# Optimization experiments

Measured on AMD Instinct MI355X. Metric: run time of the kernel, lower is better.

Reference implementation:

```python
import jax, jax.numpy as jnp
import numpy as np
from jax import lax

NUM_HOP = 2      # opt.num_hop
POOL_HOP = 1     # Encoder(..., num_hop=1) in gnn_pools
K_POOL = 1024    # int(pooling_ratio * num_patches) = 0.5 * 2048
TH = 0.0         # opt.nonzero_th
T = 0.07         # NCE temperature
NEG_FILL = -10.0


def l2norm(x):
    # Normalize(power=2): x / (sum(x^2, dim=1, keepdim)^(1/2))
    return x / jnp.sqrt(jnp.sum(x * x, axis=1, keepdims=True))


def tagconv(A, h, W, b, k):
    # DGL TAGConv: concat_{i=0..k} (D^-1/2 A D^-1/2)^i h, then linear
    deg = jnp.sum(A, axis=1)
    dinv = lax.rsqrt(jnp.maximum(deg, 1e-12))
    An = A * dinv[:, None] * dinv[None, :]   # [N,N] normalized adjacency
    feats = [h]
    for _ in range(k):
        h = An @ h
        feats.append(h)
    return jnp.concatenate(feats, axis=1) @ W + b


def nce_pair(f_t, f_s):
    # calc_gnn NCE: positives = diag(f_t . f_s); negatives = full gram with diag masked to -10
    n = f_t.shape[0]
    eye = jnp.eye(n, dtype=bool)
    pos = jnp.sum(f_t * f_s, axis=1, keepdims=True)          # [N,1]
    neg_s = jnp.where(eye, NEG_FILL, f_t @ f_s.T)            # [N,N]
    neg_t = jnp.where(eye, NEG_FILL, f_s @ f_t.T)
    out_s = jnp.concatenate([pos, neg_s], axis=1) / T
    out_t = jnp.concatenate([pos, neg_t], axis=1) / T
    # CrossEntropy with label 0 == -log_softmax(out)[:, 0], mean over rows
    loss_s = -jnp.mean(jax.nn.log_softmax(out_s, axis=1)[:, 0])
    loss_t = -jnp.mean(jax.nn.log_softmax(out_t, axis=1)[:, 0])
    return loss_s + loss_t


def setup_inputs() -> dict:
    key = jax.random.key(0)
    ks = jax.random.split(key, 8)
    N, C, D = 2048, 512, 128
    g = 0.02  # init_gain ('normal' init)
    return {
        "fs": jax.random.normal(ks[0], (N, C), jnp.float32),
        "ft": jax.random.normal(ks[1], (N, C), jnp.float32),
        "W_embed": g * jax.random.normal(ks[2], (C, D), jnp.float32),
        "b_embed": jnp.zeros((D,), jnp.float32),
        "W_gnn": g * jax.random.normal(ks[3], ((NUM_HOP + 1) * D, D), jnp.float32),
        "b_gnn": jnp.zeros((D,), jnp.float32),
        "W_pool": g * jax.random.normal(ks[4], (D, 1), jnp.float32),
        "b_pool": jnp.zeros((1,), jnp.float32),
        "W_gnnp": g * jax.random.normal(ks[5], ((POOL_HOP + 1) * D, D), jnp.float32),
        "b_gnnp": jnp.zeros((D,), jnp.float32),
    }


def reference(fs, ft, W_embed, b_embed, W_gnn, b_gnn, W_pool, b_pool, W_gnnp, b_gnnp):
    # Embed: linear + l2 norm
    f_es = l2norm(fs @ W_embed + b_embed)   # student [N, nc]
    f_et = l2norm(ft @ W_embed + b_embed)   # teacher [N, nc]

    # nonzero_graph on detached teacher features; same adjacency reused for student
    ft_d = lax.stop_gradient(f_et)
    n = f_et.shape[0]
    eye = jnp.eye(n, dtype=bool)
    A = (ft_d @ ft_d.T > TH).astype(f_et.dtype)
    A = jnp.where(eye, 1.0, A)  # dgl.add_self_loop

    # TAGConv encoder + l2norm; teacher branch detached
    f_gt = lax.stop_gradient(l2norm(tagconv(A, f_et, W_gnn, b_gnn, NUM_HOP)))
    f_gs = l2norm(tagconv(A, f_es, W_gnn, b_gnn, NUM_HOP))
    loss_g = nce_pair(f_gt, f_gs)

    # Pool / top_k_graph
    scores = jax.nn.sigmoid((f_gt @ W_pool + b_pool)[:, 0])   # [N]
    vals, idx = lax.top_k(scores, K_POOL)
    new_ht = f_gt[idx] * vals[:, None]
    new_hs = f_gs[idx] * vals[:, None]
    un = (A > 0).astype(A.dtype)
    un2 = ((un @ un) > 0).astype(A.dtype)        # 2-hop boolean adjacency
    sub = un2[idx][:, idx]                       # [k,k]
    deg = jnp.sum(sub, axis=1)
    g_pool = sub / deg[None, :]                  # replicates torch broadcast in norm_g(g/degrees)

    # pooled-stage Encoder (TAGConv k=1) on the pooled graph structure (with self loops)
    k = K_POOL
    eye_k = jnp.eye(k, dtype=bool)
    Ap = (g_pool > 0).astype(A.dtype)
    Ap = jnp.where(eye_k, 1.0, Ap)
    f_pt = lax.stop_gradient(l2norm(tagconv(Ap, new_ht, W_gnnp, b_gnnp, POOL_HOP)))
    f_ps = l2norm(tagconv(Ap, new_hs, W_gnnp, b_gnnp, POOL_HOP))
    loss_pool = nce_pair(f_pt, f_ps)

    return loss_g + loss_pool
```

## Files before the change

### kernel.cpp

```cpp
#include <hip/hip_runtime.h>


#define TINV (1.0f / 0.07f)

using short8 = __attribute__((ext_vector_type(8))) short;
using f32x4  = __attribute__((ext_vector_type(4))) float;

__device__ __forceinline__ unsigned short f2bf(float f) {
    unsigned u = __float_as_uint(f);
    u += 0x7fff + ((u >> 16) & 1);
    return (unsigned short)(u >> 16);
}

template<bool BT>
__device__ __forceinline__ void mm_tile(const float* __restrict__ A, int lda,
                                        const float* __restrict__ B, int ldb,
                                        int i0, int j0, int k0, int k1,
                                        float (&acc)[4][4],
                                        float (&As)[16][68], float (&Bs)[16][68])
{
    const int tid = threadIdx.x;
    const int tx = tid & 15;
    const int ty = tid >> 4;
    const int lr = tid >> 2;
    const int lc = (tid & 3) * 4;
    for (int k = k0; k < k1; k += 16) {
        float4 av = *(const float4*)(A + (size_t)(i0 + lr) * lda + (k + lc));
        As[lc + 0][lr] = av.x; As[lc + 1][lr] = av.y;
        As[lc + 2][lr] = av.z; As[lc + 3][lr] = av.w;
        if (BT) {
            float4 bv = *(const float4*)(B + (size_t)(j0 + lr) * ldb + (k + lc));
            Bs[lc + 0][lr] = bv.x; Bs[lc + 1][lr] = bv.y;
            Bs[lc + 2][lr] = bv.z; Bs[lc + 3][lr] = bv.w;
        } else {
            const int n = tid & 63;
            const int kb = tid >> 6;
#pragma unroll
            for (int it = 0; it < 4; ++it)
                Bs[kb * 4 + it][n] = B[(size_t)(k + kb * 4 + it) * ldb + (j0 + n)];
        }
        __syncthreads();
#pragma unroll
        for (int kk = 0; kk < 16; ++kk) {
            float a[4], b[4];
#pragma unroll
            for (int u = 0; u < 4; ++u) a[u] = As[kk][ty * 4 + u];
#pragma unroll
            for (int v = 0; v < 4; ++v) b[v] = Bs[kk][tx * 4 + v];
#pragma unroll
            for (int u = 0; u < 4; ++u)
#pragma unroll
                for (int v = 0; v < 4; ++v)
                    acc[u][v] = fmaf(a[u], b[v], acc[u][v]);
        }
        __syncthreads();
    }
}

__device__ __forceinline__ void mm64x128(const unsigned short* __restrict__ Ab, int lda,
                                         const unsigned short* __restrict__ Bb, int ldb,
                                         int i0, int j0, int k0, int Kc,
                                         f32x4 (&acc)[8],
                                         unsigned short (&As)[64][40],
                                         unsigned short (&Bs)[128][40])
{
    const int tid = threadIdx.x;
    const int w = tid >> 6;
    const int lane = tid & 63;
    const int m = lane & 15;
    const int q = lane >> 4;
    const int ar = tid >> 2;
    const int ac = (tid & 3) * 8;
    for (int ks = 0; ks < Kc; ks += 32) {
        const int k = k0 + ks;
        *(ulonglong2*)&As[ar][ac] =
            *(const ulonglong2*)(Ab + (size_t)(i0 + ar) * lda + k + ac);
        *(ulonglong2*)&Bs[ar][ac] =
            *(const ulonglong2*)(Bb + (size_t)(j0 + ar) * ldb + k + ac);
        *(ulonglong2*)&Bs[ar + 64][ac] =
            *(const ulonglong2*)(Bb + (size_t)(j0 + ar + 64) * ldb + k + ac);
        __syncthreads();
        short8 a = *(const short8*)&As[w * 16 + m][q * 8];
#pragma unroll
        for (int nt = 0; nt < 8; ++nt) {
            short8 b = *(const short8*)&Bs[nt * 16 + m][q * 8];
            acc[nt] = __builtin_amdgcn_mfma_f32_16x16x32_bf16(a, b, acc[nt], 0, 0, 0);
        }
        __syncthreads();
    }
}

__launch_bounds__(256)
__global__ void k_setup_embed(const float* __restrict__ fs, const float* __restrict__ ft,
                              const float* __restrict__ W, float* __restrict__ part,
                              size_t zstr, int* __restrict__ zwords, int zcount,
                              float* __restrict__ out,
                              const float* __restrict__ Wg, const float* __restrict__ Wp,
                              unsigned short* __restrict__ Wtall)
{
    __shared__ float As[16][68];
    __shared__ float Bs[16][68];
    const int b = blockIdx.x;
    const int tid = threadIdx.x;
    if (b < 512) {
        const int z = b & 3;
        const int by = (b >> 2) & 63;
        const int bx = b >> 8;
        const float* A = (by < 32) ? ft : fs;
        const int i0 = (by & 31) * 64;
        const int j0 = bx * 64;
        float acc[4][4] = {};
        mm_tile<false>(A, 512, W, 128, i0, j0, z * 128, z * 128 + 128, acc, As, Bs);
        const int tx = tid & 15, ty = tid >> 4;
        float* dst = part + (size_t)z * zstr;
#pragma unroll
        for (int u = 0; u < 4; ++u) {
            const size_t ri = (size_t)(by * 64 + ty * 4 + u) * 128 + j0 + tx * 4;
            float4 vv;
            vv.x = acc[u][0]; vv.y = acc[u][1]; vv.z = acc[u][2]; vv.w = acc[u][3];
            *(float4*)(dst + ri) = vv;
        }
    } else if (b < 561) {
        const int i = (b - 512) * 256 + tid;
        if (i < zcount) zwords[i] = 0;
        if (b == 512 && tid == 0) out[0] = 0.0f;
    } else {
        const int e0 = (b - 561) * 2048 + tid;
#pragma unroll
        for (int it = 0; it < 8; ++it) {
            const int e = e0 + it * 256;
            const int c = e >> 14;
            const int rem = e & 16383;
            const int n = rem >> 7, k = rem & 127;
            const float* src = (c < 3) ? (Wg + (size_t)c * 16384)
                                       : (Wp + (size_t)(c - 3) * 16384);
            Wtall[e] = f2bf(src[(size_t)k * 128 + n]);
        }
    }
}

__global__ void combine_norm(const float* __restrict__ part, int nz, size_t zstr,
                             const float* __restrict__ bias,
                             float* __restrict__ f32out,
                             unsigned short* __restrict__ bf16out)
{
    const int row = blockIdx.x;
    const int tid = threadIdx.x;
    float v = bias[tid];
    for (int z = 0; z < nz; ++z) v += part[(size_t)z * zstr + (size_t)row * 128 + tid];
    __shared__ float red[128];
    red[tid] = v * v;
    __syncthreads();
    for (int s = 64; s > 0; s >>= 1) {
        if (tid < s) red[tid] += red[tid + s];
        __syncthreads();
    }
    const float o = v * (1.0f / sqrtf(red[0]));
    f32out[(size_t)row * 128 + tid] = o;
    bf16out[(size_t)row * 128 + tid] = f2bf(o);
}

__launch_bounds__(256)
__global__ void k_gram_fused(const float* __restrict__ f_e,
                             unsigned short* __restrict__ A01,
                             unsigned long long* __restrict__ bits,
                             int* __restrict__ deg,
                             const unsigned short* __restrict__ feb,
                             const unsigned short* __restrict__ Wt,
                             float* __restrict__ hW)
{
    __shared__ __align__(16) unsigned char smem[15360];
    const int b = blockIdx.x;
    const int tid = threadIdx.x;
    if (b >= 528) {
        unsigned short (&As2)[64][40]  = *reinterpret_cast<unsigned short(*)[64][40]>(smem);
        unsigned short (&Bs2)[128][40] = *reinterpret_cast<unsigned short(*)[128][40]>(smem + 5120);
        const int lb = b - 528;
        const int z = lb >> 6;
        const int i0 = (lb & 63) * 64;
        f32x4 acc[8];
#pragma unroll
        for (int t = 0; t < 8; ++t)
#pragma unroll
            for (int r = 0; r < 4; ++r) acc[t][r] = 0.0f;
        mm64x128(feb, 128, Wt + (size_t)z * 16384, 128, i0, 0, 0, 128, acc, As2, Bs2);
        const int w = tid >> 6, lane = tid & 63, m = lane & 15, q = lane >> 4;
        float* Cb = hW + (size_t)z * (4096ull * 128);
#pragma unroll
        for (int nt = 0; nt < 8; ++nt) {
            const int col = nt * 16 + m;
#pragma unroll
            for (int r = 0; r < 4; ++r) {
                const int row = i0 + w * 16 + q * 4 + r;
                Cb[(size_t)row * 128 + col] = acc[nt][r];
            }
        }
        return;
    }
    float (&As)[16][68] = *reinterpret_cast<float(*)[16][68]>(smem);
    float (&Bs)[16][68] = *reinterpret_cast<float(*)[16][68]>(smem + 4352);
    unsigned char (&nib)[64][16]  = *reinterpret_cast<unsigned char(*)[64][16]>(smem + 8704);
    unsigned char (&nibT)[64][16] = *reinterpret_cast<unsigned char(*)[64][16]>(smem + 9728);
    unsigned long long (&chk)[64]  = *reinterpret_cast<unsigned long long(*)[64]>(smem + 10752);
    unsigned long long (&chkT)[64] = *reinterpret_cast<unsigned long long(*)[64]>(smem + 11264);
    int by = (int)((sqrtf(8.0f * b + 1.0f) - 1.0f) * 0.5f);
    while ((by + 1) * (by + 2) / 2 <= b) ++by;
    while (by * (by + 1) / 2 > b) --by;
    const int bx = b - by * (by + 1) / 2;
    const int i0 = by * 64, j0 = bx * 64;
    float acc[4][4] = {};
    mm_tile<true>(f_e, 128, f_e, 128, i0, j0, 0, 128, acc, As, Bs);
    const int tx = tid & 15, ty = tid >> 4;
    unsigned pb = 0;
#pragma unroll
    for (int u = 0; u < 4; ++u)
#pragma unroll
        for (int v = 0; v < 4; ++v) {
            bool pred = (acc[u][v] > 0.0f) || (i0 + ty * 4 + u == j0 + tx * 4 + v);
            pb |= (unsigned)pred << (u * 4 + v);
        }
#pragma unroll
    for (int u = 0; u < 4; ++u) nib[ty * 4 + u][tx] = (pb >> (4 * u)) & 15;
#pragma unroll
    for (int v = 0; v < 4; ++v) {
        unsigned nt = 0;
#pragma unroll
        for (int u = 0; u < 4; ++u) nt |= ((pb >> (u * 4 + v)) & 1u) << u;
        nibT[tx * 4 + v][ty] = nt;
    }
    __syncthreads();
    if (tid < 64) {
        unsigned long long c = 0;
#pragma unroll
        for (int t = 0; t < 16; ++t) c |= (unsigned long long)nib[tid][t] << (4 * t);
        chk[tid] = c;
        bits[(size_t)(i0 + tid) * 32 + (j0 >> 6)] = c;
        atomicAdd(&deg[i0 + tid], __popcll(c));
    } else if (tid < 128 && bx != by) {
        const int r = tid - 64;
        unsigned long long c = 0;
#pragma unroll
        for (int t = 0; t < 16; ++t) c |= (unsigned long long)nibT[r][t] << (4 * t);
        chkT[r] = c;
        bits[(size_t)(j0 + r) * 32 + (i0 >> 6)] = c;
        atomicAdd(&deg[j0 + r], __popcll(c));
    }
    __syncthreads();
#pragma unroll
    for (int it = 0; it < 4; ++it) {
        const int row = it * 16 + (tid >> 4);
        const int c0 = (tid & 15) * 4;
        unsigned short o[4];
#pragma unroll
        for (int c = 0; c < 4; ++c)
            o[c] = ((chk[row] >> (c0 + c)) & 1) ? (unsigned short)0x3F80 : (unsigned short)0;
        *(ulonglong1*)&A01[(size_t)(i0 + row) * 2048 + j0 + c0] = *(ulonglong1*)o;
        if (bx != by) {
            unsigned short o2[4];
#pragma unroll
            for (int c = 0; c < 4; ++c)
                o2[c] = ((chkT[row] >> (c0 + c)) & 1) ? (unsigned short)0x3F80 : (unsigned short)0;
            *(ulonglong1*)&A01[(size_t)(j0 + row) * 2048 + i0 + c0] = *(ulonglong1*)o2;
        }
    }
}

__launch_bounds__(256)
__global__ void mm_bf16(const unsigned short* __restrict__ A, int lda, size_t aZ,
                        const unsigned short* __restrict__ B, int ldb, size_t bZ,
                        float* __restrict__ C, int ldc, size_t cZ,
                        int Kc, int kZ)
{
    __shared__ unsigned short As[64][40];
    __shared__ unsigned short Bs[128][40];
    const int tid = threadIdx.x;
    const int bz = blockIdx.z;
    const int i0 = blockIdx.y * 64;
    const int j0 = blockIdx.x * 128;
    const int k0 = bz * kZ;
    const unsigned short* Ab = A + (size_t)bz * aZ;
    const unsigned short* Bb = B + (size_t)bz * bZ;
    float* Cb = C + (size_t)bz * cZ;
    f32x4 acc[8];
#pragma unroll
    for (int t = 0; t < 8; ++t)
#pragma unroll
        for (int r = 0; r < 4; ++r) acc[t][r] = 0.0f;
    mm64x128(Ab, lda, Bb, ldb, i0, j0, k0, Kc, acc, As, Bs);
    const int w = tid >> 6, lane = tid & 63, m = lane & 15, q = lane >> 4;
#pragma unroll
    for (int nt = 0; nt < 8; ++nt) {
        const int col = j0 + nt * 16 + m;
#pragma unroll
        for (int r = 0; r < 4; ++r) {
            const int row = i0 + w * 16 + q * 4 + r;
            Cb[(size_t)row * ldc + col] = acc[nt][r];
        }
    }
}

__global__ void reduce_xt(const float* __restrict__ part, int nz, size_t zstr,
                          int M, const float* __restrict__ dinv,
                          const float* __restrict__ addT,
                          unsigned short* __restrict__ xt)
{
    __shared__ float T[32][33];
    const int tid = threadIdx.x;
    const int iloc = tid >> 3, nq = (tid & 7) * 4;
    const int n = blockIdx.x * 32 + nq;
    const int i = blockIdx.y * 32 + iloc;
    float4 s = *(const float4*)(part + (size_t)i * 256 + n);
    for (int z = 1; z < nz; ++z) {
        float4 t = *(const float4*)(part + (size_t)z * zstr + (size_t)i * 256 + n);
        s.x += t.x; s.y += t.y; s.z += t.z; s.w += t.w;
    }
    const float d = dinv[i];
    const int srow = (n >= 128 ? M : 0) + i;
    float4 a = *(const float4*)(addT + (size_t)srow * 128 + (n & 127));
    T[nq + 0][iloc] = (a.x + s.x * d) * d;
    T[nq + 1][iloc] = (a.y + s.y * d) * d;
    T[nq + 2][iloc] = (a.z + s.z * d) * d;
    T[nq + 3][iloc] = (a.w + s.w * d) * d;
    __syncthreads();
    const int nloc = tid >> 3, ic = (tid & 7) * 4;
    unsigned short o2[4];
#pragma unroll
    for (int c = 0; c < 4; ++c) o2[c] = f2bf(T[nloc][ic + c]);
    *(ulonglong1*)(xt + (size_t)(blockIdx.x * 32 + nloc) * M + blockIdx.y * 32 + ic) =
        *(ulonglong1*)o2;
}

__global__ void combine_tag(const float* __restrict__ part, int nz, size_t zstr,
                            int Mnodes,
                            const float* __restrict__ add,
                            const float* __restrict__ dinv,
                            const float* __restrict__ bias,
                            float* __restrict__ f32out,
                            unsigned short* __restrict__ bf16out,
                            const float* __restrict__ Wp, const float* __restrict__ bp,
                            float* __restrict__ scores)
{
    const int row = blockIdx.x;
    const int tid = threadIdx.x;
    const int node = (row < Mnodes) ? row : row - Mnodes;
    const int boff = (row < Mnodes) ? 0 : 128;
    float s = 0.0f;
    for (int z = 0; z < nz; ++z)
        s += part[(size_t)z * zstr + (size_t)node * 256 + boff + tid];
    float v = bias[tid] + add[(size_t)row * 128 + tid] + dinv[node] * s;
    __shared__ float red[128];
    red[tid] = v * v;
    __syncthreads();
    for (int st = 64; st > 0; st >>= 1) {
        if (tid < st) red[tid] += red[tid + st];
        __syncthreads();
    }
    const float o = v * (1.0f / sqrtf(red[0]));
    if (f32out) f32out[(size_t)row * 128 + tid] = o;
    bf16out[(size_t)row * 128 + tid] = f2bf(o);
    if (Wp && row < Mnodes) {
        __syncthreads();
        red[tid] = o * Wp[tid];
        __syncthreads();
        for (int st = 64; st > 0; st >>= 1) {
            if (tid < st) red[tid] += red[tid + st];
            __syncthreads();
        }
        if (tid == 0) scores[row] = 1.0f / (1.0f + expf(-(red[0] + bp[0])));
    }
}

__global__ void make_xt(const float* __restrict__ src, const int* __restrict__ deg,
                        unsigned short* __restrict__ xt, float* __restrict__ dinv)
{
    __shared__ float T[32][33];
    const int b = blockIdx.x;
    const int bx = b & 7, by = b >> 3;
    const int tid = threadIdx.x;
    const int iloc = tid >> 3, nq = (tid & 7) * 4;
    const int n0 = bx * 32;
    const int i = by * 32 + iloc;
    const int srow = (n0 >= 128 ? 2048 : 0) + i;
    float4 f = *(const float4*)(src + (size_t)srow * 128 + ((n0 + nq) & 127));
    const float d = 1.0f / sqrtf((float)deg[i]);
    if (bx == 0 && (tid & 7) == 0) dinv[i] = d;
    T[nq + 0][iloc] = f.x * d; T[nq + 1][iloc] = f.y * d;
    T[nq + 2][iloc] = f.z * d; T[nq + 3][iloc] = f.w * d;
    __syncthreads();
    const int nloc = tid >> 3, ic = (tid & 7) * 4;
    unsigned short o[4];
#pragma unroll
    for (int c = 0; c < 4; ++c) o[c] = f2bf(T[nloc][ic + c]);
    *(ulonglong1*)(xt + (size_t)(n0 + nloc) * 2048 + by * 32 + ic) = *(ulonglong1*)o;
}

__launch_bounds__(256)
__global__ void k_nce_topk(const unsigned short* __restrict__ A,
                           const unsigned short* __restrict__ B,
                           float* __restrict__ rowsum, float* __restrict__ colsum,
                           float* __restrict__ pos, int gramBlocks, int bw,
                           const float* __restrict__ scores,
                           float* __restrict__ vals, int* __restrict__ idx)
{
    __shared__ unsigned short As[64][40];
    __shared__ unsigned short Bs[128][40];
    __shared__ float colbuf[4][128];
    __shared__ unsigned sv[2048];
    __shared__ int hist[256];
    __shared__ int shp, shr, sh_base, sh_out, wsum[5];
    const int tid = threadIdx.x;
    const int b = blockIdx.x;
    if (b < gramBlocks) {
        const int bx = b % bw, by = b / bw;
        const int i0 = by * 64;
        const int j0 = bx * 128;
        const int w = tid >> 6;
        const int lane = tid & 63;
        const int m = lane & 15;
        const int q = lane >> 4;
        f32x4 acc[8];
#pragma unroll
        for (int t = 0; t < 8; ++t)
#pragma unroll
            for (int r = 0; r < 4; ++r) acc[t][r] = 0.0f;
        mm64x128(A, 128, B, 128, i0, j0, 0, 128, acc, As, Bs);
        float rpart[4] = {0.0f, 0.0f, 0.0f, 0.0f};
        float cpart[8];
#pragma unroll
        for (int nt = 0; nt < 8; ++nt) {
            const int col = j0 + nt * 16 + m;
            float cs = 0.0f;
#pragma unroll
            for (int r = 0; r < 4; ++r) {
                const int row = i0 + w * 16 + q * 4 + r;
                float g = acc[nt][r];
                float e = __expf(g * TINV);
                if (row == col) { pos[row] = g; e = 0.0f; }
                rpart[r] += e;
                cs += e;
            }
            cpart[nt] = cs;
        }
#pragma unroll
        for (int r = 0; r < 4; ++r) {
            float v = rpart[r];
            v += __shfl_xor(v, 1); v += __shfl_xor(v, 2);
            v += __shfl_xor(v, 4); v += __shfl_xor(v, 8);
            if (m == 0) atomicAdd(&rowsum[i0 + w * 16 + q * 4 + r], v);
        }
#pragma unroll
        for (int nt = 0; nt < 8; ++nt) {
            float v = cpart[nt];
            v += __shfl_xor(v, 16); v += __shfl_xor(v, 32);
            if (q == 0) colbuf[w][nt * 16 + m] = v;
        }
        __syncthreads();
        if (tid < 128) {
            float v = colbuf[0][tid] + colbuf[1][tid] + colbuf[2][tid] + colbuf[3][tid];
            atomicAdd(&colsum[j0 + tid], v);
        }
    } else {
        for (int e = tid; e < 2048; e += 256) sv[e] = __float_as_uint(scores[e]);
        if (tid == 0) { shp = 0; shr = 1024; sh_base = 0; sh_out = 0; }
        __syncthreads();
        for (int byte = 3; byte >= 0; --byte) {
            hist[tid] = 0;
            __syncthreads();
            const unsigned pref = (unsigned)shp;
            const unsigned pmask = (byte == 3) ? 0u : (0xFFFFFFFFu << ((byte + 1) * 8));
            for (int e = tid; e < 2048; e += 256) {
                unsigned u = sv[e];
                if ((u & pmask) == (pref & pmask))
                    atomicAdd(&hist[(u >> (byte * 8)) & 255], 1);
            }
            __syncthreads();
            if (tid == 0) {
                int rem = shr, bs = 255;
                for (; bs > 0; --bs) {
                    if (hist[bs] >= rem) break;
                    rem -= hist[bs];
                }
                shp = (int)(pref | ((unsigned)bs << (byte * 8)));
                shr = rem;
            }
            __syncthreads();
        }
        const unsigned t = (unsigned)shp;
        const int remain = shr;
        const int lane = tid & 63, wave = tid >> 6;
        for (int pass = 0; pass < 8; ++pass) {
            const int e = pass * 256 + tid;
            const unsigned u = sv[e];
            const bool eq = (u == t);
            unsigned long long mk = __ballot(eq);
            int wpre = __popcll(mk & ((1ull << lane) - 1ull));
            if (lane == 0) wsum[wave] = __popcll(mk);
            __syncthreads();
            if (tid == 0) {
                int a = sh_base;
                for (int ww = 0; ww < 4; ++ww) { int c = wsum[ww]; wsum[ww] = a; a += c; }
                sh_base = a;
            }
            __syncthreads();
            const int rank = eq ? (wsum[wave] + wpre) : 0x7fffffff;
            if ((u > t) || (eq && rank < remain)) {
                int slot = atomicAdd(&sh_out, 1);
                idx[slot] = e;
                vals[slot] = __uint_as_float(u);
            }
            __syncthreads();
        }
    }
}

__global__ void k_final_ap(const float* __restrict__ rs, const float* __restrict__ cs,
                           const float* __restrict__ pos, float* __restrict__ out,
                           const unsigned long long* __restrict__ bits,
                           const int* __restrict__ idx,
                           unsigned short* __restrict__ Ap, int* __restrict__ degp)
{
    __shared__ unsigned long long pb[32][33];
    __shared__ unsigned long long qb[32][33];
    __shared__ float red[256];
    const int b = blockIdx.x;
    const int tid = threadIdx.x;
    if (b < 1024) {
        const int tp = (b >> 5) * 32;
        const int tq = (b & 31) * 32;
        for (int t = tid; t < 1024; t += 256) {
            int r = t >> 5, w = t & 31;
            pb[r][w] = bits[(size_t)idx[tp + r] * 32 + w];
            qb[r][w] = bits[(size_t)idx[tq + r] * 32 + w];
        }
        __syncthreads();
        const int pi = tid >> 3;
        const int qc0 = (tid & 7) * 4;
        unsigned long long a0 = 0, a1 = 0, a2 = 0, a3 = 0;
#pragma unroll
        for (int w = 0; w < 32; ++w) {
            const unsigned long long p = pb[pi][w];
            a0 |= p & qb[qc0 + 0][w];
            a1 |= p & qb[qc0 + 1][w];
            a2 |= p & qb[qc0 + 2][w];
            a3 |= p & qb[qc0 + 3][w];
        }
        unsigned short o[4] = { (unsigned short)(a0 ? 0x3F80 : 0),
                                (unsigned short)(a1 ? 0x3F80 : 0),
                                (unsigned short)(a2 ? 0x3F80 : 0),
                                (unsigned short)(a3 ? 0x3F80 : 0) };
        *(ulonglong1*)&Ap[(size_t)(tp + pi) * 1024 + tq + qc0] = *(ulonglong1*)o;
        int v = (a0 ? 1 : 0) + (a1 ? 1 : 0) + (a2 ? 1 : 0) + (a3 ? 1 : 0);
        v += __shfl_xor(v, 1); v += __shfl_xor(v, 2); v += __shfl_xor(v, 4);
        if ((tid & 7) == 0) atomicAdd(&degp[tp + pi], v);
    } else {
        const int i = (b - 1024) * 256 + tid;
        float p = pos[i] * TINV;
        float ep = __expf(p);
        float t = (logf(rs[i] + ep) - p) + (logf(cs[i] + ep) - p);
        red[tid] = t;
        __syncthreads();
        for (int s = 128; s > 0; s >>= 1) {
            if (tid < s) red[tid] += red[tid + s];
            __syncthreads();
        }
        if (tid == 0) atomicAdd(out, red[0] * (1.0f / 2048.0f));
    }
}

__global__ void nce_final(const float* __restrict__ rs, const float* __restrict__ cs,
                          const float* __restrict__ pos, float invN,
                          float* __restrict__ out)
{
    const int i = blockIdx.x * 256 + threadIdx.x;
    float p = pos[i] * TINV;
    float ep = __expf(p);
    float t = (logf(rs[i] + ep) - p) + (logf(cs[i] + ep) - p);
    __shared__ float red[256];
    red[threadIdx.x] = t;
    __syncthreads();
    for (int s = 128; s > 0; s >>= 1) {
        if (threadIdx.x < s) red[threadIdx.x] += red[threadIdx.x + s];
        __syncthreads();
    }
    if (threadIdx.x == 0) atomicAdd(out, red[0] * invN);
}

__global__ void gather_nh(const float* __restrict__ f_g, const int* __restrict__ idx,
                          const float* __restrict__ vals, const int* __restrict__ degp,
                          unsigned short* __restrict__ nhb, float* __restrict__ dinvp)
{
    const int b = blockIdx.x;
    const int tid = threadIdx.x;
    if (b < 4) {
        const int p2 = b * 256 + tid;
        dinvp[p2] = 1.0f / sqrtf((float)degp[p2]);
    }
    const int hrow = b * 8 + (tid >> 5);
    const int cq = (tid & 31) * 4;
    const int p = hrow & 1023;
    const int s = idx[p];
    const float v = vals[p];
    const int srow = (hrow >= 1024 ? 2048 : 0) + s;
    float4 f = *(const float4*)(f_g + (size_t)srow * 128 + cq);
    unsigned short o[4] = { f2bf(f.x * v), f2bf(f.y * v), f2bf(f.z * v), f2bf(f.w * v) };
    *(ulonglong1*)&nhb[(size_t)hrow * 128 + cq] = *(ulonglong1*)o;
}

__launch_bounds__(256)
__global__ void k_lin_pool(const unsigned short* __restrict__ nhb,
                           const unsigned short* __restrict__ WtP,
                           const float* __restrict__ dinvp,
                           float* __restrict__ P0,
                           unsigned short* __restrict__ Xtp)
{
    __shared__ unsigned short As[64][40];
    __shared__ unsigned short Bs[128][40];
    const int b = blockIdx.x;
    const int z = b >> 5;
    const int i0 = (b & 31) * 64;
    const int tid = threadIdx.x;
    f32x4 acc[8];
#pragma unroll
    for (int t = 0; t < 8; ++t)
#pragma unroll
        for (int r = 0; r < 4; ++r) acc[t][r] = 0.0f;
    mm64x128(nhb, 128, WtP + (size_t)z * 16384, 128, i0, 0, 0, 128, acc, As, Bs);
    const int w = tid >> 6, lane = tid & 63, m = lane & 15, q = lane >> 4;
    if (z == 0) {
#pragma unroll
        for (int nt = 0; nt < 8; ++nt) {
            const int col = nt * 16 + m;
#pragma unroll
            for (int r = 0; r < 4; ++r) {
                const int row = i0 + w * 16 + q * 4 + r;
                P0[(size_t)row * 128 + col] = acc[nt][r];
            }
        }
    } else {
        const int boff = (i0 >= 1024) ? 128 : 0;
        const int p0 = (i0 & 1023) + w * 16 + q * 4;
        float4 dv = *(const float4*)(dinvp + p0);
        const float dvr[4] = { dv.x, dv.y, dv.z, dv.w };
#pragma unroll
        for (int nt = 0; nt < 8; ++nt) {
            const int n = boff + nt * 16 + m;
            unsigned short o[4];
#pragma unroll
            for (int r = 0; r < 4; ++r) o[r] = f2bf(acc[nt][r] * dvr[r]);
            *(ulonglong1*)&Xtp[(size_t)n * 1024 + p0] = *(ulonglong1*)o;
        }
    }
}

extern "C" void kernel_launch(void* const* d_in, const int* in_sizes, int n_in,
                              void* d_out, int out_size, void* d_ws, size_t ws_size,
                              hipStream_t stream)
{
    (void)in_sizes; (void)n_in; (void)out_size; (void)ws_size;
    const float* fs      = (const float*)d_in[0];
    const float* ft      = (const float*)d_in[1];
    const float* W_embed = (const float*)d_in[2];
    const float* b_embed = (const float*)d_in[3];
    const float* W_gnn   = (const float*)d_in[4];
    const float* b_gnn   = (const float*)d_in[5];
    const float* W_pool  = (const float*)d_in[6];
    const float* b_pool  = (const float*)d_in[7];
    const float* W_gnnp  = (const float*)d_in[8];
    const float* b_gnnp  = (const float*)d_in[9];
    float* out = (float*)d_out;

    float* ws = (float*)d_ws;
    size_t o = 0;
    auto alloc = [&](size_t n) { float* p = ws + o; o += (n + 3) & ~3ull; return p; };
    float* bigB   = alloc(2048ull * 2048);
    float* f_e    = alloc(4096 * 128);
    float* f_g    = alloc(4096 * 128);
    unsigned short* A01  = (unsigned short*)alloc(2048ull * 2048 / 2);
    unsigned short* feb  = (unsigned short*)alloc(4096ull * 128 / 2);
    unsigned short* Xt1  = (unsigned short*)alloc(256ull * 2048 / 2);
    unsigned short* Xt2  = (unsigned short*)alloc(256ull * 2048 / 2);
    unsigned short* f_gb = (unsigned short*)alloc(4096ull * 128 / 2);
    unsigned short* Wtall= (unsigned short*)alloc(5ull * 16384 / 2);
    unsigned short* Ap01 = (unsigned short*)alloc(1024ull * 1024 / 2);
    unsigned short* nhb  = (unsigned short*)alloc(2048ull * 128 / 2);
    unsigned short* Xtp  = (unsigned short*)alloc(256ull * 1024 / 2);
    unsigned short* f_pb = (unsigned short*)alloc(2048ull * 128 / 2);
    float* hW     = alloc(3ull * 4096 * 128);
    float* P0     = alloc(2048ull * 128);
    float* dinv   = alloc(2048);
    float* scores = alloc(2048);
    float* vals   = alloc(1024);
    int*   idxb   = (int*)alloc(1024);
    float* dinvp  = alloc(1024);
    unsigned long long* bits = (unsigned long long*)alloc(2048 * 32 * 2);
    float* nceb = alloc(9216);
    int*   deg  = (int*)alloc(2048);
    int*   degp = (int*)alloc(1024);
    const int kZeroCount = 9216 + 2048 + 1024;

    const size_t FSTR = 4096ull * 128;
    const size_t PSTR = 1024ull * 256;
    unsigned short* Wt  = Wtall;
    unsigned short* WtP = Wtall + 3ull * 16384;
    float* hW0 = hW;
    float* hW1 = hW + FSTR;
    float* hW2 = hW + 2 * FSTR;
    float* rs  = nceb;
    float* csu = nceb + 2048;
    float* pos = nceb + 4096;
    float* rsp  = nceb + 6144;
    float* csp  = nceb + 7168;
    float* posp = nceb + 8192;

    k_setup_embed<<<601, 256, 0, stream>>>(fs, ft, W_embed, bigB, FSTR,
                                           (int*)nceb, kZeroCount, out, W_gnn, W_gnnp, Wtall);
    combine_norm<<<4096, 128, 0, stream>>>(bigB, 4, FSTR, b_embed, f_e, feb);
    k_gram_fused<<<720, 256, 0, stream>>>(f_e, A01, bits, deg, feb, Wt, hW);
    make_xt<<<512, 256, 0, stream>>>(hW2, deg, Xt1, dinv);
    mm_bf16<<<dim3(2, 32, 4), 256, 0, stream>>>(A01, 2048, 0, Xt1, 2048, 0,
                                                bigB, 256, FSTR, 512, 512);
    reduce_xt<<<dim3(8, 64), 256, 0, stream>>>(bigB, 4, FSTR, 2048, dinv, hW1, Xt2);
    mm_bf16<<<dim3(2, 32, 4), 256, 0, stream>>>(A01, 2048, 0, Xt2, 2048, 0,
                                                bigB, 256, FSTR, 512, 512);
    combine_tag<<<4096, 128, 0, stream>>>(bigB, 4, FSTR, 2048, hW0, dinv, b_gnn,
                                          f_g, f_gb, W_pool, b_pool, scores);
    k_nce_topk<<<513, 256, 0, stream>>>(f_gb, f_gb + 2048 * 128, rs, csu, pos,
                                        512, 16, scores, vals, idxb);
    k_final_ap<<<1032, 256, 0, stream>>>(rs, csu, pos, out, bits, idxb, Ap01, degp);
    gather_nh<<<256, 256, 0, stream>>>(f_g, idxb, vals, degp, nhb, dinvp);
    k_lin_pool<<<64, 256, 0, stream>>>(nhb, WtP, dinvp, P0, Xtp);
    mm_bf16<<<dim3(2, 16, 4), 256, 0, stream>>>(Ap01, 1024, 0, Xtp, 1024, 0,
                                                bigB, 256, PSTR, 256, 256);
    combine_tag<<<2048, 128, 0, stream>>>(bigB, 4, PSTR, 1024, P0, dinvp, b_gnnp,
                                          nullptr, f_pb, nullptr, nullptr, nullptr);
    k_nce_topk<<<128, 256, 0, stream>>>(f_pb, f_pb + 1024 * 128, rsp, csp, posp,
                                        128, 8, nullptr, nullptr, nullptr);
    nce_final<<<4, 256, 0, stream>>>(rsp, csp, posp, 1.0f / 1024.0f, out);
}
```

Measured before the change: 208.3 us.

## Fuse hop matmuls with epilogues and drop split-K partial buffers

Replaces the split-K mm_bf16 plus reduce/combine kernel pairs with full-K 16-row-tile matmul kernels. Their epilogues apply the normalization, the l2norm and the pool score, or write the transposed bf16 next-hop input directly. It also folds the gather into k_lin_pool, computes inverse sqrt degrees inline, and does the final NCE reduction in the last gram block through an atomic counter. This removes several launches and fp32 partial round-trips through global memory. The cost is lower per-block parallelism, with each block running a serial 2048-long K loop using only two MFMA tiles per wave.

```diff
diff --git a/kernel.cpp b/kernel.cpp
--- a/kernel.cpp
+++ b/kernel.cpp
@@ -265,111 +265,6 @@
     }
 }
 
-__launch_bounds__(256)
-__global__ void mm_bf16(const unsigned short* __restrict__ A, int lda, size_t aZ,
-                        const unsigned short* __restrict__ B, int ldb, size_t bZ,
-                        float* __restrict__ C, int ldc, size_t cZ,
-                        int Kc, int kZ)
-{
-    __shared__ unsigned short As[64][40];
-    __shared__ unsigned short Bs[128][40];
-    const int tid = threadIdx.x;
-    const int bz = blockIdx.z;
-    const int i0 = blockIdx.y * 64;
-    const int j0 = blockIdx.x * 128;
-    const int k0 = bz * kZ;
-    const unsigned short* Ab = A + (size_t)bz * aZ;
-    const unsigned short* Bb = B + (size_t)bz * bZ;
-    float* Cb = C + (size_t)bz * cZ;
-    f32x4 acc[8];
-#pragma unroll
-    for (int t = 0; t < 8; ++t)
-#pragma unroll
-        for (int r = 0; r < 4; ++r) acc[t][r] = 0.0f;
-    mm64x128(Ab, lda, Bb, ldb, i0, j0, k0, Kc, acc, As, Bs);
-    const int w = tid >> 6, lane = tid & 63, m = lane & 15, q = lane >> 4;
-#pragma unroll
-    for (int nt = 0; nt < 8; ++nt) {
-        const int col = j0 + nt * 16 + m;
-#pragma unroll
-        for (int r = 0; r < 4; ++r) {
-            const int row = i0 + w * 16 + q * 4 + r;
-            Cb[(size_t)row * ldc + col] = acc[nt][r];
-        }
-    }
-}
-
-__global__ void reduce_xt(const float* __restrict__ part, int nz, size_t zstr,
-                          int M, const float* __restrict__ dinv,
-                          const float* __restrict__ addT,
-                          unsigned short* __restrict__ xt)
-{
-    __shared__ float T[32][33];
-    const int tid = threadIdx.x;
-    const int iloc = tid >> 3, nq = (tid & 7) * 4;
-    const int n = blockIdx.x * 32 + nq;
-    const int i = blockIdx.y * 32 + iloc;
-    float4 s = *(const float4*)(part + (size_t)i * 256 + n);
-    for (int z = 1; z < nz; ++z) {
-        float4 t = *(const float4*)(part + (size_t)z * zstr + (size_t)i * 256 + n);
-        s.x += t.x; s.y += t.y; s.z += t.z; s.w += t.w;
-    }
-    const float d = dinv[i];
-    const int srow = (n >= 128 ? M : 0) + i;
-    float4 a = *(const float4*)(addT + (size_t)srow * 128 + (n & 127));
-    T[nq + 0][iloc] = (a.x + s.x * d) * d;
-    T[nq + 1][iloc] = (a.y + s.y * d) * d;
-    T[nq + 2][iloc] = (a.z + s.z * d) * d;
-    T[nq + 3][iloc] = (a.w + s.w * d) * d;
-    __syncthreads();
-    const int nloc = tid >> 3, ic = (tid & 7) * 4;
-    unsigned short o2[4];
-#pragma unroll
-    for (int c = 0; c < 4; ++c) o2[c] = f2bf(T[nloc][ic + c]);
-    *(ulonglong1*)(xt + (size_t)(blockIdx.x * 32 + nloc) * M + blockIdx.y * 32 + ic) =
-        *(ulonglong1*)o2;
-}
-
-__global__ void combine_tag(const float* __restrict__ part, int nz, size_t zstr,
-                            int Mnodes,
-                            const float* __restrict__ add,
-                            const float* __restrict__ dinv,
-                            const float* __restrict__ bias,
-                            float* __restrict__ f32out,
-                            unsigned short* __restrict__ bf16out,
-                            const float* __restrict__ Wp, const float* __restrict__ bp,
-                            float* __restrict__ scores)
-{
-    const int row = blockIdx.x;
-    const int tid = threadIdx.x;
-    const int node = (row < Mnodes) ? row : row - Mnodes;
-    const int boff = (row < Mnodes) ? 0 : 128;
-    float s = 0.0f;
-    for (int z = 0; z < nz; ++z)
-        s += part[(size_t)z * zstr + (size_t)node * 256 + boff + tid];
-    float v = bias[tid] + add[(size_t)row * 128 + tid] + dinv[node] * s;
-    __shared__ float red[128];
-    red[tid] = v * v;
-    __syncthreads();
-    for (int st = 64; st > 0; st >>= 1) {
-        if (tid < st) red[tid] += red[tid + st];
-        __syncthreads();
-    }
-    const float o = v * (1.0f / sqrtf(red[0]));
-    if (f32out) f32out[(size_t)row * 128 + tid] = o;
-    bf16out[(size_t)row * 128 + tid] = f2bf(o);
-    if (Wp && row < Mnodes) {
-        __syncthreads();
-        red[tid] = o * Wp[tid];
-        __syncthreads();
-        for (int st = 64; st > 0; st >>= 1) {
-            if (tid < st) red[tid] += red[tid + st];
-            __syncthreads();
-        }
-        if (tid == 0) scores[row] = 1.0f / (1.0f + expf(-(red[0] + bp[0])));
-    }
-}
-
 __global__ void make_xt(const float* __restrict__ src, const int* __restrict__ deg,
                         unsigned short* __restrict__ xt, float* __restrict__ dinv)
 {
@@ -395,12 +290,203 @@
 }
 
 __launch_bounds__(256)
+__global__ void k_hop_xt2(const unsigned short* __restrict__ A,
+                          const unsigned short* __restrict__ X,
+                          const float* __restrict__ dinv,
+                          const float* __restrict__ hW1,
+                          unsigned short* __restrict__ xt2)
+{
+    __shared__ unsigned short As[16][40];
+    __shared__ unsigned short Bs[128][40];
+    __shared__ unsigned short T[128][24];
+    __shared__ float sd[16];
+    const int tid = threadIdx.x;
+    const int bx = blockIdx.x;
+    const int i0 = blockIdx.y * 16;
+    const int j0 = bx * 128;
+    const int w = tid >> 6, lane = tid & 63, m = lane & 15, q = lane >> 4;
+    if (tid < 16) sd[tid] = dinv[i0 + tid];
+    const int aru = tid >> 4, acu = (tid & 15) * 2;
+    const int br = tid >> 1, bc = (tid & 1) * 16;
+    const unsigned short* Apt = A + (size_t)(i0 + aru) * 2048 + acu;
+    const unsigned short* Bpt = X + (size_t)(j0 + br) * 2048 + bc;
+    unsigned aReg = *(const unsigned*)Apt;
+    ulonglong2 bReg0 = *(const ulonglong2*)Bpt;
+    ulonglong2 bReg1 = *(const ulonglong2*)(Bpt + 8);
+    f32x4 acc[2];
+#pragma unroll
+    for (int t = 0; t < 2; ++t)
+#pragma unroll
+        for (int r = 0; r < 4; ++r) acc[t][r] = 0.0f;
+    for (int ks = 0; ks < 2048; ks += 32) {
+        *(unsigned*)&As[aru][acu] = aReg;
+        *(ulonglong2*)&Bs[br][bc] = bReg0;
+        *(ulonglong2*)&Bs[br][bc + 8] = bReg1;
+        __syncthreads();
+        if (ks + 32 < 2048) {
+            aReg = *(const unsigned*)(Apt + ks + 32);
+            bReg0 = *(const ulonglong2*)(Bpt + ks + 32);
+            bReg1 = *(const ulonglong2*)(Bpt + ks + 32 + 8);
+        }
+        short8 a = *(const short8*)&As[m][q * 8];
+#pragma unroll
+        for (int nt = 0; nt < 2; ++nt) {
+            short8 bb = *(const short8*)&Bs[w * 32 + nt * 16 + m][q * 8];
+            acc[nt] = __builtin_amdgcn_mfma_f32_16x16x32_bf16(a, bb, acc[nt], 0, 0, 0);
+        }
+        __syncthreads();
+    }
+#pragma unroll
+    for (int nt = 0; nt < 2; ++nt) {
+        const int nl = w * 32 + nt * 16 + m;
+        const int n = j0 + nl;
+        const size_t boff = (n >= 128) ? 2048 : 0;
+#pragma unroll
+        for (int r = 0; r < 4; ++r) {
+            const int il = q * 4 + r;
+            const float d = sd[il];
+            const float hv = hW1[(boff + i0 + il) * 128 + (n & 127)];
+            T[nl][il] = f2bf((hv + d * acc[nt][r]) * d);
+        }
+    }
+    __syncthreads();
+    const int nl2 = tid >> 1, ic = (tid & 1) * 8;
+    *(ulonglong2*)(xt2 + (size_t)(j0 + nl2) * 2048 + i0 + ic) =
+        *(const ulonglong2*)&T[nl2][ic];
+}
+
+__launch_bounds__(256)
+__global__ void k_hop_norm(const unsigned short* __restrict__ A, int Kc,
+                           const unsigned short* __restrict__ X,
+                           const float* __restrict__ addP,
+                           const float* __restrict__ bias,
+                           const float* __restrict__ dinvf,
+                           const int* __restrict__ degi,
+                           float* __restrict__ f32out,
+                           unsigned short* __restrict__ bf16out,
+                           const float* __restrict__ Wp, const float* __restrict__ bp,
+                           float* __restrict__ scores)
+{
+    __shared__ unsigned short As[16][40];
+    __shared__ unsigned short Bs[128][40];
+    __shared__ float sd[16];
+    __shared__ float redA[4][16];
+    __shared__ float redB[4][16];
+    const int tid = threadIdx.x;
+    const int bx = blockIdx.x;
+    const int i0 = blockIdx.y * 16;
+    const int j0 = bx * 128;
+    const int w = tid >> 6, lane = tid & 63, m = lane & 15, q = lane >> 4;
+    if (tid < 16) sd[tid] = degi ? rsqrtf((float)degi[i0 + tid]) : dinvf[i0 + tid];
+    const int aru = tid >> 4, acu = (tid & 15) * 2;
+    const int br = tid >> 1, bc = (tid & 1) * 16;
+    const unsigned short* Apt = A + (size_t)(i0 + aru) * Kc + acu;
+    const unsigned short* Bpt = X + (size_t)(j0 + br) * Kc + bc;
+    unsigned aReg = *(const unsigned*)Apt;
+    ulonglong2 bReg0 = *(const ulonglong2*)Bpt;
+    ulonglong2 bReg1 = *(const ulonglong2*)(Bpt + 8);
+    f32x4 acc[2];
+#pragma unroll
+    for (int t = 0; t < 2; ++t)
+#pragma unroll
+        for (int r = 0; r < 4; ++r) acc[t][r] = 0.0f;
+    for (int ks = 0; ks < Kc; ks += 32) {
+        *(unsigned*)&As[aru][acu] = aReg;
+        *(ulonglong2*)&Bs[br][bc] = bReg0;
+        *(ulonglong2*)&Bs[br][bc + 8] = bReg1;
+        __syncthreads();
+        if (ks + 32 < Kc) {
+            aReg = *(const unsigned*)(Apt + ks + 32);
+            bReg0 = *(const ulonglong2*)(Bpt + ks + 32);
+            bReg1 = *(const ulonglong2*)(Bpt + ks + 32 + 8);
+        }
+        short8 a = *(const short8*)&As[m][q * 8];
+#pragma unroll
+        for (int nt = 0; nt < 2; ++nt) {
+            short8 bb = *(const short8*)&Bs[w * 32 + nt * 16 + m][q * 8];
+            acc[nt] = __builtin_amdgcn_mfma_f32_16x16x32_bf16(a, bb, acc[nt], 0, 0, 0);
+        }
+        __syncthreads();
+    }
+    float pre[2][4];
+    float ssr[4] = {0.0f, 0.0f, 0.0f, 0.0f};
+#pragma unroll
+    for (int nt = 0; nt < 2; ++nt) {
+        const int col = w * 32 + nt * 16 + m;
+        const float bv = bias[col];
+#pragma unroll
+        for (int r = 0; r < 4; ++r) {
+            const int il = q * 4 + r;
+            const size_t srow = (size_t)bx * Kc + i0 + il;
+            const float v = bv + addP[srow * 128 + col] + sd[il] * acc[nt][r];
+            pre[nt][r] = v;
+            ssr[r] += v * v;
+        }
+    }
+#pragma unroll
+    for (int r = 0; r < 4; ++r) {
+        float v = ssr[r];
+        v += __shfl_xor(v, 1); v += __shfl_xor(v, 2);
+        v += __shfl_xor(v, 4); v += __shfl_xor(v, 8);
+        ssr[r] = v;
+    }
+    if (m == 0) {
+#pragma unroll
+        for (int r = 0; r < 4; ++r) redA[w][q * 4 + r] = ssr[r];
+    }
+    __syncthreads();
+    float nf[4];
+#pragma unroll
+    for (int r = 0; r < 4; ++r) {
+        const int il = q * 4 + r;
+        nf[r] = rsqrtf(redA[0][il] + redA[1][il] + redA[2][il] + redA[3][il]);
+    }
+    const bool doSc = (scores != nullptr) && (bx == 0);
+    float scp[4] = {0.0f, 0.0f, 0.0f, 0.0f};
+#pragma unroll
+    for (int nt = 0; nt < 2; ++nt) {
+        const int col = w * 32 + nt * 16 + m;
+        const float wv = doSc ? Wp[col] : 0.0f;
+#pragma unroll
+        for (int r = 0; r < 4; ++r) {
+            const int il = q * 4 + r;
+            const size_t srow = (size_t)bx * Kc + i0 + il;
+            const float o = pre[nt][r] * nf[r];
+            if (f32out) f32out[srow * 128 + col] = o;
+            bf16out[srow * 128 + col] = f2bf(o);
+            scp[r] = fmaf(o, wv, scp[r]);
+        }
+    }
+    if (doSc) {
+#pragma unroll
+        for (int r = 0; r < 4; ++r) {
+            float v = scp[r];
+            v += __shfl_xor(v, 1); v += __shfl_xor(v, 2);
+            v += __shfl_xor(v, 4); v += __shfl_xor(v, 8);
+            scp[r] = v;
+        }
+        if (m == 0) {
+#pragma unroll
+            for (int r = 0; r < 4; ++r) redB[w][q * 4 + r] = scp[r];
+        }
+        __syncthreads();
+        if (tid < 16) {
+            const float s = redB[0][tid] + redB[1][tid] + redB[2][tid] + redB[3][tid]
+                          + bp[0];
+            scores[i0 + tid] = 1.0f / (1.0f + expf(-s));
+        }
+    }
+}
+
+__launch_bounds__(256)
 __global__ void k_nce_topk(const unsigned short* __restrict__ A,
                            const unsigned short* __restrict__ B,
                            float* __restrict__ rowsum, float* __restrict__ colsum,
                            float* __restrict__ pos, int gramBlocks, int bw,
                            const float* __restrict__ scores,
-                           float* __restrict__ vals, int* __restrict__ idx)
+                           float* __restrict__ vals, int* __restrict__ idx,
+                           int* __restrict__ counter, float* __restrict__ outT,
+                           float invN, int nRows)
 {
     __shared__ unsigned short As[64][40];
     __shared__ unsigned short Bs[128][40];
@@ -408,6 +494,7 @@
     __shared__ unsigned sv[2048];
     __shared__ int hist[256];
     __shared__ int shp, shr, sh_base, sh_out, wsum[5];
+    __shared__ int lastFlag;
     const int tid = threadIdx.x;
     const int b = blockIdx.x;
     if (b < gramBlocks) {
@@ -458,6 +545,29 @@
         if (tid < 128) {
             float v = colbuf[0][tid] + colbuf[1][tid] + colbuf[2][tid] + colbuf[3][tid];
             atomicAdd(&colsum[j0 + tid], v);
+        }
+        if (counter) {
+            __threadfence();
+            __syncthreads();
+            if (tid == 0) lastFlag = (atomicAdd(counter, 1) == gramBlocks - 1);
+            __syncthreads();
+            if (lastFlag) {
+                __threadfence();
+                float accl = 0.0f;
+                for (int i = tid; i < nRows; i += 256) {
+                    float p = pos[i] * TINV;
+                    float ep = __expf(p);
+                    accl += (logf(rowsum[i] + ep) - p) + (logf(colsum[i] + ep) - p);
+                }
+                float* red = (float*)colbuf;
+                red[tid] = accl;
+                __syncthreads();
+                for (int s = 128; s > 0; s >>= 1) {
+                    if (tid < s) red[tid] += red[tid + s];
+                    __syncthreads();
+                }
+                if (tid == 0) atomicAdd(outT, red[0] * invN);
+            }
         }
     } else {
         for (int e = tid; e < 2048; e += 256) sv[e] = __float_as_uint(scores[e]);
@@ -567,51 +677,11 @@
     }
 }
 
-__global__ void nce_final(const float* __restrict__ rs, const float* __restrict__ cs,
-                          const float* __restrict__ pos, float invN,
-                          float* __restrict__ out)
-{
-    const int i = blockIdx.x * 256 + threadIdx.x;
-    float p = pos[i] * TINV;
-    float ep = __expf(p);
-    float t = (logf(rs[i] + ep) - p) + (logf(cs[i] + ep) - p);
-    __shared__ float red[256];
-    red[threadIdx.x] = t;
-    __syncthreads();
-    for (int s = 128; s > 0; s >>= 1) {
-        if (threadIdx.x < s) red[threadIdx.x] += red[threadIdx.x + s];
-        __syncthreads();
-    }
-    if (threadIdx.x == 0) atomicAdd(out, red[0] * invN);
-}
-
-__global__ void gather_nh(const float* __restrict__ f_g, const int* __restrict__ idx,
-                          const float* __restrict__ vals, const int* __restrict__ degp,
-                          unsigned short* __restrict__ nhb, float* __restrict__ dinvp)
-{
-    const int b = blockIdx.x;
-    const int tid = threadIdx.x;
-    if (b < 4) {
-        const int p2 = b * 256 + tid;
-        dinvp[p2] = 1.0f / sqrtf((float)degp[p2]);
-    }
-    const int hrow = b * 8 + (tid >> 5);
-    const int cq = (tid & 31) * 4;
-    const int p = hrow & 1023;
-    const int s = idx[p];
-    const float v = vals[p];
-    const int srow = (hrow >= 1024 ? 2048 : 0) + s;
-    float4 f = *(const float4*)(f_g + (size_t)srow * 128 + cq);
-    unsigned short o[4] = { f2bf(f.x * v), f2bf(f.y * v), f2bf(f.z * v), f2bf(f.w * v) };
-    *(ulonglong1*)&nhb[(size_t)hrow * 128 + cq] = *(ulonglong1*)o;
-}
-
 __launch_bounds__(256)
-__global__ void k_lin_pool(const unsigned short* __restrict__ nhb,
+__global__ void k_lin_pool(const float* __restrict__ f_g, const int* __restrict__ idx,
+                           const float* __restrict__ vals, const int* __restrict__ degp,
                            const unsigned short* __restrict__ WtP,
-                           const float* __restrict__ dinvp,
-                           float* __restrict__ P0,
-                           unsigned short* __restrict__ Xtp)
+                           float* __restrict__ P0, unsigned short* __restrict__ Xtp)
 {
     __shared__ unsigned short As[64][40];
     __shared__ unsigned short Bs[128][40];
@@ -619,13 +689,41 @@
     const int z = b >> 5;
     const int i0 = (b & 31) * 64;
     const int tid = threadIdx.x;
+    const int w = tid >> 6, lane = tid & 63, m = lane & 15, q = lane >> 4;
+    const int ar = tid >> 2, ac = (tid & 3) * 8;
+    const int hrow = i0 + ar;
+    const int p = hrow & 1023;
+    const int s = idx[p];
+    const float v = vals[p];
+    const size_t srow = (size_t)((hrow >= 1024) ? 2048 : 0) + s;
+    const int br = tid >> 1, bc = (tid & 1) * 16;
     f32x4 acc[8];
 #pragma unroll
     for (int t = 0; t < 8; ++t)
 #pragma unroll
         for (int r = 0; r < 4; ++r) acc[t][r] = 0.0f;
-    mm64x128(nhb, 128, WtP + (size_t)z * 16384, 128, i0, 0, 0, 128, acc, As, Bs);
-    const int w = tid >> 6, lane = tid & 63, m = lane & 15, q = lane >> 4;
+    for (int ks = 0; ks < 128; ks += 32) {
+        float4 f1 = *(const float4*)(f_g + srow * 128 + ks + ac);
+        float4 f2 = *(const float4*)(f_g + srow * 128 + ks + ac + 4);
+        short8 pk;
+        pk[0] = (short)f2bf(f1.x * v); pk[1] = (short)f2bf(f1.y * v);
+        pk[2] = (short)f2bf(f1.z * v); pk[3] = (short)f2bf(f1.w * v);
+        pk[4] = (short)f2bf(f2.x * v); pk[5] = (short)f2bf(f2.y * v);
+        pk[6] = (short)f2bf(f2.z * v); pk[7] = (short)f2bf(f2.w * v);
+        *(short8*)&As[ar][ac] = pk;
+        *(ulonglong2*)&Bs[br][bc] =
+            *(const ulonglong2*)(WtP + (size_t)z * 16384 + (size_t)br * 128 + ks + bc);
+        *(ulonglong2*)&Bs[br][bc + 8] =
+            *(const ulonglong2*)(WtP + (size_t)z * 16384 + (size_t)br * 128 + ks + bc + 8);
+        __syncthreads();
+        short8 a = *(const short8*)&As[w * 16 + m][q * 8];
+#pragma unroll
+        for (int nt = 0; nt < 8; ++nt) {
+            short8 bb = *(const short8*)&Bs[nt * 16 + m][q * 8];
+            acc[nt] = __builtin_amdgcn_mfma_f32_16x16x32_bf16(a, bb, acc[nt], 0, 0, 0);
+        }
+        __syncthreads();
+    }
     if (z == 0) {
 #pragma unroll
         for (int nt = 0; nt < 8; ++nt) {
@@ -639,8 +737,9 @@
     } else {
         const int boff = (i0 >= 1024) ? 128 : 0;
         const int p0 = (i0 & 1023) + w * 16 + q * 4;
-        float4 dv = *(const float4*)(dinvp + p0);
-        const float dvr[4] = { dv.x, dv.y, dv.z, dv.w };
+        int4 dg = *(const int4*)(degp + p0);
+        const float dvr[4] = { rsqrtf((float)dg.x), rsqrtf((float)dg.y),
+                               rsqrtf((float)dg.z), rsqrtf((float)dg.w) };
 #pragma unroll
         for (int nt = 0; nt < 8; ++nt) {
             const int n = boff + nt * 16 + m;
@@ -682,7 +781,6 @@
     unsigned short* f_gb = (unsigned short*)alloc(4096ull * 128 / 2);
     unsigned short* Wtall= (unsigned short*)alloc(5ull * 16384 / 2);
     unsigned short* Ap01 = (unsigned short*)alloc(1024ull * 1024 / 2);
-    unsigned short* nhb  = (unsigned short*)alloc(2048ull * 128 / 2);
     unsigned short* Xtp  = (unsigned short*)alloc(256ull * 1024 / 2);
     unsigned short* f_pb = (unsigned short*)alloc(2048ull * 128 / 2);
     float* hW     = alloc(3ull * 4096 * 128);
@@ -691,15 +789,14 @@
     float* scores = alloc(2048);
     float* vals   = alloc(1024);
     int*   idxb   = (int*)alloc(1024);
-    float* dinvp  = alloc(1024);
     unsigned long long* bits = (unsigned long long*)alloc(2048 * 32 * 2);
     float* nceb = alloc(9216);
     int*   deg  = (int*)alloc(2048);
     int*   degp = (int*)alloc(1024);
-    const int kZeroCount = 9216 + 2048 + 1024;
+    int*   cnt  = (int*)alloc(4);
+    const int kZeroCount = 9216 + 2048 + 1024 + 4;
 
     const size_t FSTR = 4096ull * 128;
-    const size_t PSTR = 1024ull * 256;
     unsigned short* Wt  = Wtall;
     unsigned short* WtP = Wtall + 3ull * 16384;
     float* hW0 = hW;
@@ -717,23 +814,19 @@
     combine_norm<<<4096, 128, 0, stream>>>(bigB, 4, FSTR, b_embed, f_e, feb);
     k_gram_fused<<<720, 256, 0, stream>>>(f_e, A01, bits, deg, feb, Wt, hW);
     make_xt<<<512, 256, 0, stream>>>(hW2, deg, Xt1, dinv);
-    mm_bf16<<<dim3(2, 32, 4), 256, 0, stream>>>(A01, 2048, 0, Xt1, 2048, 0,
-                                                bigB, 256, FSTR, 512, 512);
-    reduce_xt<<<dim3(8, 64), 256, 0, stream>>>(bigB, 4, FSTR, 2048, dinv, hW1, Xt2);
-    mm_bf16<<<dim3(2, 32, 4), 256, 0, stream>>>(A01, 2048, 0, Xt2, 2048, 0,
-                                                bigB, 256, FSTR, 512, 512);
-    combine_tag<<<4096, 128, 0, stream>>>(bigB, 4, FSTR, 2048, hW0, dinv, b_gnn,
-                                          f_g, f_gb, W_pool, b_pool, scores);
+    k_hop_xt2<<<dim3(2, 128), 256, 0, stream>>>(A01, Xt1, dinv, hW1, Xt2);
+    k_hop_norm<<<dim3(2, 128), 256, 0, stream>>>(A01, 2048, Xt2, hW0, b_gnn,
+                                                 dinv, nullptr, f_g, f_gb,
+                                                 W_pool, b_pool, scores);
     k_nce_topk<<<513, 256, 0, stream>>>(f_gb, f_gb + 2048 * 128, rs, csu, pos,
-                                        512, 16, scores, vals, idxb);
+                                        512, 16, scores, vals, idxb,
+                                        nullptr, nullptr, 0.0f, 0);
     k_final_ap<<<1032, 256, 0, stream>>>(rs, csu, pos, out, bits, idxb, Ap01, degp);
-    gather_nh<<<256, 256, 0, stream>>>(f_g, idxb, vals, degp, nhb, dinvp);
-    k_lin_pool<<<64, 256, 0, stream>>>(nhb, WtP, dinvp, P0, Xtp);
-    mm_bf16<<<dim3(2, 16, 4), 256, 0, stream>>>(Ap01, 1024, 0, Xtp, 1024, 0,
-                                                bigB, 256, PSTR, 256, 256);
-    combine_tag<<<2048, 128, 0, stream>>>(bigB, 4, PSTR, 1024, P0, dinvp, b_gnnp,
-                                          nullptr, f_pb, nullptr, nullptr, nullptr);
+    k_lin_pool<<<64, 256, 0, stream>>>(f_g, idxb, vals, degp, WtP, P0, Xtp);
+    k_hop_norm<<<dim3(2, 64), 256, 0, stream>>>(Ap01, 1024, Xtp, P0, b_gnnp,
+                                                nullptr, degp, nullptr, f_pb,
+                                                nullptr, nullptr, nullptr);
     k_nce_topk<<<128, 256, 0, stream>>>(f_pb, f_pb + 1024 * 128, rsp, csp, posp,
-                                        128, 8, nullptr, nullptr, nullptr);
-    nce_final<<<4, 256, 0, stream>>>(rsp, csp, posp, 1.0f / 1024.0f, out);
-}
+                                        128, 8, nullptr, nullptr, nullptr,
+                                        cnt, out, 1.0f / 1024.0f, 1024);
+}
```

Result: slower. 232.8 us (+11.8%).
